# Performance work log

Hardware: AMD Instinct MI355X
Metric: run time of the kernel (lower is better)

The kernel has to match this reference:

```python
import jax, jax.numpy as jnp
import numpy as np

B, L, C, F, K = 16, 512, 384, 384, 3
MAX_DUR = 8
MEL_MAX = L * MAX_DUR  # fixed expanded length (padded/masked)
PAD = (K - 1) // 2


def conv1d(x, w, b):
    # x: [B, T, C] ; w: [F, C, K] ; 'same' padding as Conv1d(padding=(K-1)//2)
    y = jax.lax.conv_general_dilated(x.transpose(0, 2, 1), w, (1,), [(PAD, PAD)],
                                     dimension_numbers=('NCH', 'OIH', 'NCH'))
    return y.transpose(0, 2, 1) + b


def layernorm(x, g, b, eps=1e-5):
    mu = jnp.mean(x, axis=-1, keepdims=True)
    var = jnp.mean(jnp.square(x - mu), axis=-1, keepdims=True)
    return (x - mu) * jax.lax.rsqrt(var + eps) * g + b


def predictor(x, w1, b1, g1, be1, w2, b2, g2, be2, wl, bl):
    # Conv -> ReLU -> LN -> (Dropout=id) -> Conv -> ReLU -> LN -> Linear(F,1)
    h = layernorm(jax.nn.relu(conv1d(x, w1, b1)), g1, be1)
    h = layernorm(jax.nn.relu(conv1d(h, w2, b2)), g2, be2)
    return h @ wl + bl  # [B, T, 1]


def length_regulate(x, dur):
    # gather/repeat-interleave form of the dense one-hot alignment matmul
    cum = jnp.cumsum(dur, axis=-1)                       # [B, L]
    t = jnp.arange(MEL_MAX)                              # [T]
    idx = (t[None, :, None] >= cum[:, None, :]).sum(-1)  # [B, T] frame->phoneme
    idx = jnp.minimum(idx, x.shape[1] - 1)
    out = jnp.take_along_axis(x, idx[..., None], axis=1)  # [B, T, C]
    mask = (t[None, :] < cum[:, -1:]).astype(x.dtype)      # zero padded frames
    return out * mask[..., None]


def _pred_params(key, prefix):
    ks = jax.random.split(key, 4)
    s = 0.05
    return {
        f'{prefix}_w1': jax.random.normal(ks[0], (F, C, K), jnp.float32) * s,
        f'{prefix}_b1': jnp.zeros((F,), jnp.float32),
        f'{prefix}_g1': jnp.ones((F,), jnp.float32),
        f'{prefix}_be1': jnp.zeros((F,), jnp.float32),
        f'{prefix}_w2': jax.random.normal(ks[1], (F, F, K), jnp.float32) * s,
        f'{prefix}_b2': jnp.zeros((F,), jnp.float32),
        f'{prefix}_g2': jnp.ones((F,), jnp.float32),
        f'{prefix}_be2': jnp.zeros((F,), jnp.float32),
        f'{prefix}_wl': jax.random.normal(ks[2], (F, 1), jnp.float32) * s,
        f'{prefix}_bl': jnp.zeros((1,), jnp.float32),
    }


def setup_inputs() -> dict:
    key = jax.random.key(0)
    kx, kd, k1, k2, k3 = jax.random.split(key, 5)
    inp = {'x': jax.random.normal(kx, (B, L, C), jnp.float32)}
    inp.update(_pred_params(k1, 'dp'))
    inp.update(_pred_params(k2, 'pp'))
    inp.update(_pred_params(k3, 'ep'))
    inp['dur'] = jax.random.randint(kd, (B, L), 0, MAX_DUR, jnp.int32)
    return inp


def reference(x,
              dp_w1, dp_b1, dp_g1, dp_be1, dp_w2, dp_b2, dp_g2, dp_be2, dp_wl, dp_bl,
              pp_w1, pp_b1, pp_g1, pp_be1, pp_w2, pp_b2, pp_g2, pp_be2, pp_wl, pp_bl,
              ep_w1, ep_b1, ep_g1, ep_be1, ep_w2, ep_b2, ep_g2, ep_be2, ep_wl, ep_bl,
              dur):
    durations = predictor(x, dp_w1, dp_b1, dp_g1, dp_be1, dp_w2, dp_b2, dp_g2, dp_be2, dp_wl, dp_bl)
    expanded = length_regulate(x, dur)                    # [B, MEL_MAX, C]
    pitches = predictor(expanded, pp_w1, pp_b1, pp_g1, pp_be1, pp_w2, pp_b2, pp_g2, pp_be2, pp_wl, pp_bl)
    out = expanded + pitches
    energies = predictor(out, ep_w1, ep_b1, ep_g1, ep_be1, ep_w2, ep_b2, ep_g2, ep_be2, ep_wl, ep_bl)
    out = out + energies
    return (out, durations, pitches, energies)
```

## Files before the change

### kernel.cpp

```cpp
#include <hip/hip_runtime.h>
#include <stdint.h>
#include <stdio.h>

#define BB   16
#define LL   512
#define CC   384
#define FF   384
#define KW   3
#define MEL  4096
#define KKT  (CC*KW)

#define O_OUT 0
#define N_OUT (BB*MEL*CC)
#define O_DUR (N_OUT)
#define O_PIT (O_DUR + BB*LL)
#define O_EN  (O_PIT + BB*MEL)

using bf16x8 = __attribute__((ext_vector_type(8))) short;
using f32x4  = __attribute__((ext_vector_type(4))) float;

__device__ __forceinline__ unsigned short f2bf(float v) {
    union { float f; unsigned int u; } cv; cv.f = v;
    unsigned int u = cv.u;
    u += 0x7FFFu + ((u >> 16) & 1u);
    return (unsigned short)(u >> 16);
}
__device__ __forceinline__ float bf2f(unsigned short u) {
    union { unsigned int u; float f; } cv; cv.u = ((unsigned int)u) << 16; return cv.f;
}

__device__ __forceinline__ void gld_lds16(const unsigned short* gp, unsigned short* lp) {
    __builtin_amdgcn_global_load_lds(
        (const __attribute__((address_space(1))) unsigned int*)gp,
        (__attribute__((address_space(3))) unsigned int*)lp, 16, 0, 0);
}

__global__ void wtrans_kernel(const float* __restrict__ w, unsigned short* __restrict__ wt2) {
    int i = blockIdx.x * 256 + threadIdx.x;
    if (i >= FF * KKT) return;
    const int t = i / 24576;
    const int r = i - t * 24576;
    const int c = r >> 3;
    const int e = r & 7;
    const int q = c / 384;
    const int bn = c - q * 384;
    const int kk = t * 64 + q * 8 + e;
    const int k = kk / CC;
    const int ch = kk - k * CC;
    wt2[i] = f2bf(w[(size_t)bn * KKT + ch * KW + k]);
}

__global__ void convert_x_kernel(const float* __restrict__ x, unsigned short* __restrict__ o) {
    int i = blockIdx.x * 256 + threadIdx.x;
    if (i >= BB * LL * CC) return;
    int b = i / (LL * CC);
    int r = i - b * (LL * CC);
    int t = r / CC;
    int c = r - t * CC;
    o[((size_t)b * (LL + 2) + t + 1) * CC + c] = f2bf(x[i]);
}

__global__ void zpad_kernel(unsigned short* __restrict__ buf, int T) {
    int b = blockIdx.x >> 1;
    int w = blockIdx.x & 1;
    size_t row = (size_t)b * (T + 2) + (w ? (T + 1) : 0);
    buf[row * CC + threadIdx.x] = 0;
}

template<int T, bool FL>
__global__ __launch_bounds__(512)
void conv_ln_kernel(const unsigned short* __restrict__ inb,
                    const unsigned short* __restrict__ wt2,
                    const float* __restrict__ bias,
                    const float* __restrict__ g,
                    const float* __restrict__ be,
                    unsigned short* __restrict__ outb,
                    const float* __restrict__ wl,
                    const float* __restrict__ bl,
                    float* __restrict__ op) {
    __shared__ __align__(16) unsigned short LDS[2][32768];

    constexpr int NT = KKT / 64;
    const int m0 = blockIdx.x * 128;
    const int b  = m0 / T;
    const int t0 = m0 - b * T;
    const int tid  = threadIdx.x;
    const int lane = tid & 63;
    const int wv   = tid >> 6;
    const int wr   = wv >> 2;
    const int wc   = wv & 3;

    const int rowS = tid >> 3;
    const int gch  = (tid & 7) ^ (rowS & 7);
    const unsigned short* srcA0 =
        inb + ((size_t)b * (T + 2) + t0 + rowS) * CC + gch * 8;
    const unsigned short* srcA1 =
        inb + ((size_t)b * (T + 2) + t0 + 64 + rowS) * CC + gch * 8;
    const unsigned short* srcB = wt2 + (size_t)tid * 8;

    f32x4 acc[4][6] = {};

    auto stage = [&](int bi, int t) {
        const int offA = t * 64;
        gld_lds16(srcA0 + offA, &LDS[bi][(wv * 64) * 8]);
        gld_lds16(srcA1 + offA, &LDS[bi][(512 + wv * 64) * 8]);
        const size_t offB = (size_t)t * 24576;
        #pragma unroll
        for (int s = 0; s < 6; ++s)
            gld_lds16(srcB + offB + s * 4096,
                      &LDS[bi][8192 + (s * 512 + wv * 64) * 8]);
    };

    auto compute = [&](int bi) {
        const int q0 = lane >> 4;
        const int l15 = lane & 15;
        __builtin_amdgcn_s_setprio(1);
        #pragma unroll
        for (int kk = 0; kk < 2; ++kk) {
            bf16x8 af[4], bf[6];
            const int q = 4 * kk + q0;
            const int ca = q ^ (lane & 7);
            #pragma unroll
            for (int i = 0; i < 4; ++i) {
                const int ar = wr * 64 + i * 16 + l15;
                af[i] = *reinterpret_cast<const bf16x8*>(&LDS[bi][(ar * 8 + ca) * 8]);
            }
            #pragma unroll
            for (int j = 0; j < 6; ++j) {
                const int bn = wc * 96 + j * 16 + l15;
                bf[j] = *reinterpret_cast<const bf16x8*>(&LDS[bi][8192 + (q * 384 + bn) * 8]);
            }
            #pragma unroll
            for (int i = 0; i < 4; ++i)
                #pragma unroll
                for (int j = 0; j < 6; ++j)
                    acc[i][j] = __builtin_amdgcn_mfma_f32_16x16x32_bf16(
                        af[i], bf[j], acc[i][j], 0, 0, 0);
        }
        __builtin_amdgcn_s_setprio(0);
    };

    stage(0, 0);
    stage(1, 1);

    #pragma unroll 2
    for (int t = 0; t < NT; ++t) {
        asm volatile("s_waitcnt vmcnt(8)" ::: "memory");
        __builtin_amdgcn_s_barrier();
        asm volatile("" ::: "memory");
        compute(t & 1);
        asm volatile("" ::: "memory");
        __builtin_amdgcn_s_barrier();
        int nt_ = t + 2; if (nt_ > NT - 1) nt_ = NT - 1;
        stage(t & 1, nt_);
    }
    asm volatile("s_waitcnt vmcnt(0)" ::: "memory");
    __syncthreads();

    const int colb = wc * 96 + (lane & 15);
    float b6[6];
    #pragma unroll
    for (int j = 0; j < 6; ++j) b6[j] = bias[colb + j * 16];
    #pragma unroll
    for (int i = 0; i < 4; ++i)
        #pragma unroll
        for (int j = 0; j < 6; ++j)
            #pragma unroll
            for (int r = 0; r < 4; ++r) {
                float v = acc[i][j][r] + b6[j];
                acc[i][j][r] = v > 0.f ? v : 0.f;
            }

    float S1[4][4], S2[4][4];
    #pragma unroll
    for (int i = 0; i < 4; ++i)
        #pragma unroll
        for (int r = 0; r < 4; ++r) {
            float s = 0.f, s2 = 0.f;
            #pragma unroll
            for (int j = 0; j < 6; ++j) { const float v = acc[i][j][r]; s += v; s2 += v * v; }
            #pragma unroll
            for (int m = 1; m <= 8; m <<= 1) { s += __shfl_xor(s, m); s2 += __shfl_xor(s2, m); }
            S1[i][r] = s; S2[i][r] = s2;
        }

    float2* red = (float2*)&LDS[0][0];
    if ((lane & 15) == 0) {
        const int q = lane >> 4;
        #pragma unroll
        for (int i = 0; i < 4; ++i)
            #pragma unroll
            for (int r = 0; r < 4; ++r)
                red[(wr * 64 + i * 16 + q * 4 + r) * 4 + wc] = make_float2(S1[i][r], S2[i][r]);
    }
    __syncthreads();

    float g6[6], be6[6];
    #pragma unroll
    for (int j = 0; j < 6; ++j) { g6[j] = g[colb + j * 16]; be6[j] = be[colb + j * 16]; }

    if (!FL) {
        #pragma unroll
        for (int i = 0; i < 4; ++i)
            #pragma unroll
            for (int r = 0; r < 4; ++r) {
                const int row = wr * 64 + i * 16 + (lane >> 4) * 4 + r;
                const float2 p0 = red[row * 4 + 0], p1 = red[row * 4 + 1];
                const float2 p2 = red[row * 4 + 2], p3 = red[row * 4 + 3];
                const float S = p0.x + p1.x + p2.x + p3.x;
                const float Q = p0.y + p1.y + p2.y + p3.y;
                const float mu = S * (1.f / 384.f);
                const float rs = rsqrtf(Q * (1.f / 384.f) - mu * mu + 1e-5f);
                unsigned short* qp = outb + ((size_t)b * (T + 2) + t0 + row + 1) * CC + colb;
                #pragma unroll
                for (int j = 0; j < 6; ++j)
                    qp[j * 16] = f2bf((acc[i][j][r] - mu) * rs * g6[j] + be6[j]);
            }
    } else {
        float wl6[6];
        #pragma unroll
        for (int j = 0; j < 6; ++j) wl6[j] = wl[colb + j * 16];
        float* redl = (float*)&LDS[1][0];
        #pragma unroll
        for (int i = 0; i < 4; ++i)
            #pragma unroll
            for (int r = 0; r < 4; ++r) {
                const int row = wr * 64 + i * 16 + (lane >> 4) * 4 + r;
                const float2 p0 = red[row * 4 + 0], p1 = red[row * 4 + 1];
                const float2 p2 = red[row * 4 + 2], p3 = red[row * 4 + 3];
                const float S = p0.x + p1.x + p2.x + p3.x;
                const float Q = p0.y + p1.y + p2.y + p3.y;
                const float mu = S * (1.f / 384.f);
                const float rs = rsqrtf(Q * (1.f / 384.f) - mu * mu + 1e-5f);
                float sl = 0.f;
                #pragma unroll
                for (int j = 0; j < 6; ++j)
                    sl += ((acc[i][j][r] - mu) * rs * g6[j] + be6[j]) * wl6[j];
                #pragma unroll
                for (int m = 1; m <= 8; m <<= 1) sl += __shfl_xor(sl, m);
                if ((lane & 15) == 0) redl[row * 4 + wc] = sl;
            }
        __syncthreads();
        if (tid < 128)
            op[m0 + tid] = redl[tid * 4] + redl[tid * 4 + 1] +
                           redl[tid * 4 + 2] + redl[tid * 4 + 3] + bl[0];
    }
}

__global__ void cumsum_kernel(const int* __restrict__ dur, int* __restrict__ cum) {
    __shared__ int s[LL];
    const int b = blockIdx.x, t = threadIdx.x;
    s[t] = dur[b * LL + t];
    __syncthreads();
    for (int off = 1; off < LL; off <<= 1) {
        int v = (t >= off) ? s[t - off] : 0;
        __syncthreads();
        s[t] += v;
        __syncthreads();
    }
    cum[b * LL + t] = s[t];
}

__global__ void idx_kernel(const int* __restrict__ cum, int* __restrict__ idxm) {
    const int i = blockIdx.x * 256 + threadIdx.x;
    if (i >= BB * MEL) return;
    const int b = i / MEL, t = i - b * MEL;
    const int* cb = cum + b * LL;
    const int total = cb[LL - 1];
    int lo = 0, hi = LL;
    while (lo < hi) {
        const int mid = (lo + hi) >> 1;
        if (cb[mid] <= t) lo = mid + 1; else hi = mid;
    }
    int id = lo > LL - 1 ? LL - 1 : lo;
    idxm[i] = (t < total) ? id : -1;
}

__global__ void gather_kernel(const float* __restrict__ x, const int* __restrict__ idxm,
                              unsigned short* __restrict__ bb0) {
    const int i = blockIdx.x * 256 + threadIdx.x;
    const int row = i / 96;
    const int c4  = (i - row * 96) * 4;
    const int b = row >> 12, t = row & (MEL - 1);
    const int id = idxm[row];
    float4 v = make_float4(0.f, 0.f, 0.f, 0.f);
    if (id >= 0) v = *(const float4*)(x + ((size_t)b * LL + id) * CC + c4);
    uint2 pk;
    pk.x = (unsigned int)f2bf(v.x) | ((unsigned int)f2bf(v.y) << 16);
    pk.y = (unsigned int)f2bf(v.z) | ((unsigned int)f2bf(v.w) << 16);
    *(uint2*)(bb0 + ((size_t)b * (MEL + 2) + t + 1) * CC + c4) = pk;
}

__global__ void addp_kernel(const unsigned short* __restrict__ bb0,
                            const float* __restrict__ pv,
                            unsigned short* __restrict__ be0) {
    const int i = blockIdx.x * 256 + threadIdx.x;
    const int row = i / 48;
    const int c8  = (i - row * 48) * 8;
    const int b = row >> 12, t = row & (MEL - 1);
    const float p = pv[row];
    const size_t o = ((size_t)b * (MEL + 2) + t + 1) * CC + c8;
    const uint4 in = *(const uint4*)(bb0 + o);
    uint4 ot;
    const unsigned int w[4] = {in.x, in.y, in.z, in.w};
    unsigned int r[4];
    #pragma unroll
    for (int k = 0; k < 4; ++k) {
        const float lo = bf2f((unsigned short)w[k]) + p;
        const float hi = bf2f((unsigned short)(w[k] >> 16)) + p;
        r[k] = (unsigned int)f2bf(lo) | ((unsigned int)f2bf(hi) << 16);
    }
    ot.x = r[0]; ot.y = r[1]; ot.z = r[2]; ot.w = r[3];
    *(uint4*)(be0 + o) = ot;
}

__global__ void final_kernel(const float* __restrict__ x, const int* __restrict__ idxm,
                             const float* __restrict__ pv, const float* __restrict__ ev,
                             float* __restrict__ out0) {
    const int i = blockIdx.x * 256 + threadIdx.x;
    const int row = i / 96;
    const int c4  = (i - row * 96) * 4;
    const int b = row >> 12;
    const int id = idxm[row];
    const float add = pv[row] + ev[row];
    float4 v = make_float4(0.f, 0.f, 0.f, 0.f);
    if (id >= 0) v = *(const float4*)(x + ((size_t)b * LL + id) * CC + c4);
    v.x += add; v.y += add; v.z += add; v.w += add;
    *(float4*)(out0 + (size_t)row * CC + c4) = v;
}

extern "C" void kernel_launch(void* const* d_in, const int* in_sizes, int n_in,
                              void* d_out, int out_size, void* d_ws, size_t ws_size,
                              hipStream_t stream) {
    const float* x = (const float*)d_in[0];
    const float* P[30];
    for (int i = 0; i < 30; ++i) P[i] = (const float*)d_in[1 + i];
    const int* dur = (const int*)d_in[31];
    float* out = (float*)d_out;

    char* ws = (char*)d_ws;
    const size_t WTT_ELEMS = (size_t)FF * KKT;
    const size_t WTT_BYTES = WTT_ELEMS * 2;
    unsigned short* wtt[6];
    for (int i = 0; i < 6; ++i) wtt[i] = (unsigned short*)(ws + i * WTT_BYTES);
    int* cum  = (int*)(ws + 5308416);
    int* idxm = (int*)(ws + 5341184);
    unsigned short* sb0 = (unsigned short*)(ws + 5603328);
    unsigned short* h1s = (unsigned short*)(ws + 11919360);
    unsigned short* bb0 = (unsigned short*)(ws + 18235392);
    unsigned short* h1p = (unsigned short*)(ws + 68616192);
    unsigned short* be0 = (unsigned short*)(ws + 118996992);
    const size_t need = 169377792;
    if (ws_size < need)
        fprintf(stderr, "kernel_launch: ws too small: %zu < %zu\n", ws_size, need);

    const float *dp_w1=P[0], *dp_b1=P[1], *dp_g1=P[2], *dp_be1=P[3], *dp_w2=P[4],
                *dp_b2=P[5], *dp_g2=P[6], *dp_be2=P[7], *dp_wl=P[8], *dp_bl=P[9];
    const float *pp_w1=P[10], *pp_b1=P[11], *pp_g1=P[12], *pp_be1=P[13], *pp_w2=P[14],
                *pp_b2=P[15], *pp_g2=P[16], *pp_be2=P[17], *pp_wl=P[18], *pp_bl=P[19];
    const float *ep_w1=P[20], *ep_b1=P[21], *ep_g1=P[22], *ep_be1=P[23], *ep_w2=P[24],
                *ep_b2=P[25], *ep_g2=P[26], *ep_be2=P[27], *ep_wl=P[28], *ep_bl=P[29];

    const int wtg = (int)((WTT_ELEMS + 255) / 256);
    wtrans_kernel<<<wtg, 256, 0, stream>>>(dp_w1, wtt[0]);
    wtrans_kernel<<<wtg, 256, 0, stream>>>(dp_w2, wtt[1]);
    wtrans_kernel<<<wtg, 256, 0, stream>>>(pp_w1, wtt[2]);
    wtrans_kernel<<<wtg, 256, 0, stream>>>(pp_w2, wtt[3]);
    wtrans_kernel<<<wtg, 256, 0, stream>>>(ep_w1, wtt[4]);
    wtrans_kernel<<<wtg, 256, 0, stream>>>(ep_w2, wtt[5]);

    convert_x_kernel<<<(BB * LL * CC + 255) / 256, 256, 0, stream>>>(x, sb0);
    zpad_kernel<<<BB * 2, CC, 0, stream>>>(sb0, LL);
    zpad_kernel<<<BB * 2, CC, 0, stream>>>(h1s, LL);
    zpad_kernel<<<BB * 2, CC, 0, stream>>>(bb0, MEL);
    zpad_kernel<<<BB * 2, CC, 0, stream>>>(h1p, MEL);
    zpad_kernel<<<BB * 2, CC, 0, stream>>>(be0, MEL);

    cumsum_kernel<<<BB, LL, 0, stream>>>(dur, cum);
    idx_kernel<<<(BB * MEL + 255) / 256, 256, 0, stream>>>(cum, idxm);

    conv_ln_kernel<LL, false><<<BB * LL / 128, 512, 0, stream>>>(
        sb0, wtt[0], dp_b1, dp_g1, dp_be1, h1s, nullptr, nullptr, nullptr);
    conv_ln_kernel<LL, true><<<BB * LL / 128, 512, 0, stream>>>(
        h1s, wtt[1], dp_b2, dp_g2, dp_be2, nullptr, dp_wl, dp_bl, out + O_DUR);

    gather_kernel<<<BB * MEL * 96 / 256, 256, 0, stream>>>(x, idxm, bb0);

    conv_ln_kernel<MEL, false><<<BB * MEL / 128, 512, 0, stream>>>(
        bb0, wtt[2], pp_b1, pp_g1, pp_be1, h1p, nullptr, nullptr, nullptr);
    conv_ln_kernel<MEL, true><<<BB * MEL / 128, 512, 0, stream>>>(
        h1p, wtt[3], pp_b2, pp_g2, pp_be2, nullptr, pp_wl, pp_bl, out + O_PIT);

    addp_kernel<<<BB * MEL * 48 / 256, 256, 0, stream>>>(bb0, out + O_PIT, be0);

    conv_ln_kernel<MEL, false><<<BB * MEL / 128, 512, 0, stream>>>(
        be0, wtt[4], ep_b1, ep_g1, ep_be1, h1p, nullptr, nullptr, nullptr);
    conv_ln_kernel<MEL, true><<<BB * MEL / 128, 512, 0, stream>>>(
        h1p, wtt[5], ep_b2, ep_g2, ep_be2, nullptr, ep_wl, ep_bl, out + O_EN);

    final_kernel<<<BB * MEL * 96 / 256, 256, 0, stream>>>(
        x, idxm, out + O_PIT, out + O_EN, out + O_OUT);
}
```

Measured before the change: 431.7 us.

## Load conv weights directly into registers and shrink LDS to A-only ring

The B (weight) tiles are no longer staged through LDS. Each wave now loads its weight fragments straight from global memory into registers, double-buffered across the two K halves. LDS holds only the A activation tiles in a 4-deep ring with one barrier per iteration, which cuts LDS footprint and LDS traffic and may allow more blocks per CU. In exchange, weight reads become redundant per-wave global/L2 loads, and the software pipeline relies on hand-placed vmcnt waits, so ordering bugs or load-latency stalls are a risk.

```diff
diff --git a/kernel.cpp b/kernel.cpp
--- a/kernel.cpp
+++ b/kernel.cpp
@@ -78,7 +78,7 @@
                     const float* __restrict__ wl,
                     const float* __restrict__ bl,
                     float* __restrict__ op) {
-    __shared__ __align__(16) unsigned short LDS[2][32768];
+    __shared__ __align__(16) unsigned short LDS[4][8192];
 
     constexpr int NT = KKT / 64;
     const int m0 = blockIdx.x * 128;
@@ -89,6 +89,8 @@
     const int wv   = tid >> 6;
     const int wr   = wv >> 2;
     const int wc   = wv & 3;
+    const int q0   = lane >> 4;
+    const int l15  = lane & 15;
 
     const int rowS = tid >> 3;
     const int gch  = (tid & 7) ^ (rowS & 7);
@@ -96,63 +98,60 @@
         inb + ((size_t)b * (T + 2) + t0 + rowS) * CC + gch * 8;
     const unsigned short* srcA1 =
         inb + ((size_t)b * (T + 2) + t0 + 64 + rowS) * CC + gch * 8;
-    const unsigned short* srcB = wt2 + (size_t)tid * 8;
+    const unsigned short* wtb0 = wt2 + (size_t)((q0)     * 384 + wc * 96 + l15) * 8;
+    const unsigned short* wtb1 = wt2 + (size_t)((4 + q0) * 384 + wc * 96 + l15) * 8;
 
     f32x4 acc[4][6] = {};
-
-    auto stage = [&](int bi, int t) {
-        const int offA = t * 64;
-        gld_lds16(srcA0 + offA, &LDS[bi][(wv * 64) * 8]);
-        gld_lds16(srcA1 + offA, &LDS[bi][(512 + wv * 64) * 8]);
-        const size_t offB = (size_t)t * 24576;
-        #pragma unroll
-        for (int s = 0; s < 6; ++s)
-            gld_lds16(srcB + offB + s * 4096,
-                      &LDS[bi][8192 + (s * 512 + wv * 64) * 8]);
+    bf16x8 bA[6], bB[6];
+
+    auto stageA = [&](int bi, int t) {
+        const int off = t * 64;
+        gld_lds16(srcA0 + off, &LDS[bi][wv * 512]);
+        gld_lds16(srcA1 + off, &LDS[bi][4096 + wv * 512]);
     };
-
-    auto compute = [&](int bi) {
-        const int q0 = lane >> 4;
-        const int l15 = lane & 15;
+    auto loadB0 = [&](int t) {
+        const unsigned short* p = wtb0 + (size_t)t * 24576;
+        #pragma unroll
+        for (int j = 0; j < 6; ++j) bA[j] = *(const bf16x8*)(p + j * 128);
+    };
+    auto loadB1 = [&](int t) {
+        const unsigned short* p = wtb1 + (size_t)t * 24576;
+        #pragma unroll
+        for (int j = 0; j < 6; ++j) bB[j] = *(const bf16x8*)(p + j * 128);
+    };
+    auto computeK = [&](int bi, int kkq, const bf16x8* br) {
+        bf16x8 af[4];
+        const int ca = kkq ^ (lane & 7);
+        #pragma unroll
+        for (int i = 0; i < 4; ++i) {
+            const int ar = wr * 64 + i * 16 + l15;
+            af[i] = *(const bf16x8*)(&LDS[bi][ar * 64 + ca * 8]);
+        }
         __builtin_amdgcn_s_setprio(1);
         #pragma unroll
-        for (int kk = 0; kk < 2; ++kk) {
-            bf16x8 af[4], bf[6];
-            const int q = 4 * kk + q0;
-            const int ca = q ^ (lane & 7);
-            #pragma unroll
-            for (int i = 0; i < 4; ++i) {
-                const int ar = wr * 64 + i * 16 + l15;
-                af[i] = *reinterpret_cast<const bf16x8*>(&LDS[bi][(ar * 8 + ca) * 8]);
-            }
-            #pragma unroll
-            for (int j = 0; j < 6; ++j) {
-                const int bn = wc * 96 + j * 16 + l15;
-                bf[j] = *reinterpret_cast<const bf16x8*>(&LDS[bi][8192 + (q * 384 + bn) * 8]);
-            }
-            #pragma unroll
-            for (int i = 0; i < 4; ++i)
-                #pragma unroll
-                for (int j = 0; j < 6; ++j)
-                    acc[i][j] = __builtin_amdgcn_mfma_f32_16x16x32_bf16(
-                        af[i], bf[j], acc[i][j], 0, 0, 0);
-        }
+        for (int i = 0; i < 4; ++i)
+            #pragma unroll
+            for (int j = 0; j < 6; ++j)
+                acc[i][j] = __builtin_amdgcn_mfma_f32_16x16x32_bf16(
+                    af[i], br[j], acc[i][j], 0, 0, 0);
         __builtin_amdgcn_s_setprio(0);
     };
 
-    stage(0, 0);
-    stage(1, 1);
-
-    #pragma unroll 2
+    stageA(0, 0);
+    loadB0(0);
+    stageA(1, 1);
+    asm volatile("s_waitcnt vmcnt(8)" ::: "memory");
+
     for (int t = 0; t < NT; ++t) {
-        asm volatile("s_waitcnt vmcnt(8)" ::: "memory");
         __builtin_amdgcn_s_barrier();
         asm volatile("" ::: "memory");
-        compute(t & 1);
-        asm volatile("" ::: "memory");
-        __builtin_amdgcn_s_barrier();
-        int nt_ = t + 2; if (nt_ > NT - 1) nt_ = NT - 1;
-        stage(t & 1, nt_);
+        loadB1(t);
+        stageA((t + 2) & 3, (t + 2 > NT - 1) ? NT - 1 : t + 2);
+        asm volatile("s_waitcnt vmcnt(8)" ::: "memory");
+        computeK(t & 3, q0, bA);
+        loadB0((t + 1 > NT - 1) ? NT - 1 : t + 1);
+        asm volatile("s_waitcnt vmcnt(8)" ::: "memory");
+        computeK(t & 3, 4 + q0, bB);
     }
     asm volatile("s_waitcnt vmcnt(0)" ::: "memory");
     __syncthreads();
```

Result: slower. 449.9 us (+4.2%).
